# Kernel tuning notes

Measured on AMD Instinct MI355X. Metric: run time of the kernel, lower is better.

Reference implementation:

```python
import jax, jax.numpy as jnp
import numpy as np

NF, NH1, NH21, NH22, NCLS = 6, 128, 128, 128, 3
OBS_X, OBS_Y, OBS_Z, R = 10.0, 10.0, 9.0, 7.0
BATCH = 131072


def setup_inputs() -> dict:
    key = jax.random.key(0)
    ks = jax.random.split(key, 16)
    def lin(kw, kb, fan_in, fan_out):
        bound = 1.0 / np.sqrt(fan_in)
        w = jax.random.uniform(kw, (fan_out, fan_in), jnp.float32, -bound, bound)
        b = jax.random.uniform(kb, (fan_out,), jnp.float32, -bound, bound)
        return w, b
    fc1_w, fc1_b = lin(ks[0], ks[1], NF, NH1)
    fc21_w, fc21_b = lin(ks[2], ks[3], NH1, NH21)
    fc22_w, fc22_b = lin(ks[4], ks[5], NH1, NH22)
    fcm1_w, fcm1_b = lin(ks[6], ks[7], NH21, NH21)
    fcm2_w, fcm2_b = lin(ks[8], ks[9], NH22, NH22)
    fc31_w, fc31_b = lin(ks[10], ks[11], NH21, NCLS)
    fc32_w, fc32_b = lin(ks[12], ks[13], NH22, 2)
    x = jax.random.normal(ks[14], (BATCH, NF), jnp.float32)
    mean = jnp.array([10.0, 0.0, 10.0, 0.0, 9.0, 0.0], jnp.float32)
    std = jnp.array([5.0, 2.0, 5.0, 2.0, 5.0, 2.0], jnp.float32)
    return {"x": x, "mean": mean, "std": std,
            "fc1_w": fc1_w, "fc1_b": fc1_b,
            "fc21_w": fc21_w, "fc21_b": fc21_b,
            "fc22_w": fc22_w, "fc22_b": fc22_b,
            "fcm1_w": fcm1_w, "fcm1_b": fcm1_b,
            "fcm2_w": fcm2_w, "fcm2_b": fcm2_b,
            "fc31_w": fc31_w, "fc31_b": fc31_b,
            "fc32_w": fc32_w, "fc32_b": fc32_b,
            "sgn": 1}


def _forward(x, mean, std, fc1_w, fc1_b, fc21_w, fc21_b, fc22_w, fc22_b,
             fcm1_w, fcm1_b, fcm2_w, fcm2_b, fc31_w, fc31_b, fc32_w, fc32_b):
    x0 = x * std + mean                                   # de-normalized state [B,6]
    h = jnp.tanh(x @ fc1_w.T + fc1_b)                     # [B,NH1]
    x21 = jnp.tanh(h @ fc21_w.T + fc21_b)
    x22 = jnp.tanh(h @ fc22_w.T + fc22_b)
    x21 = jnp.tanh(x21 @ fcm1_w.T + fcm1_b)
    x22 = jnp.tanh(x22 @ fcm2_w.T + fcm2_b)
    x31 = x21 @ fc31_w.T + fc31_b                         # QP linear term p, [B,3]
    x32 = 4.0 * jax.nn.sigmoid(x22 @ fc32_w.T + fc32_b)   # HOCBF penalties, [B,2]

    # higher-order CBF terms
    px, vx, py, vy, pz, vz = (x0[:, i] for i in range(6))
    dx, dy, dz = px - OBS_X, py - OBS_Y, pz - OBS_Z
    barrier = dx**4 + dy**4 + dz**4 - R**4
    barrier_dot = 4.0 * (dx**3 * vx + dy**3 * vy + dz**3 * vz)
    Lf2b = 12.0 * (dx**2 * vx**2 + dy**2 * vy**2 + dz**2 * vz**2)
    G = -4.0 * jnp.stack([dx**3, dy**3, dz**3], axis=-1)  # [B,3], single constraint G u <= h
    hvec = Lf2b + (x32[:, 0] + x32[:, 1]) * barrier_dot + x32[:, 0] * x32[:, 1] * barrier  # [B]

    # QP: min 0.5 u^T u + x31^T u  s.t.  G u <= h  (Q = I, one constraint)
    # Closed-form KKT: u = -x31 - lam*G, lam = max(0, (G @ (-x31) - h) / (G @ G))
    u_unc = -x31
    Gu = jnp.sum(G * u_unc, axis=-1)                      # [B]
    GG = jnp.sum(G * G, axis=-1)                          # [B]
    lam = jnp.maximum(Gu - hvec, 0.0) / GG
    u = u_unc - lam[:, None] * G                          # [B,3]
    return u


def reference(x, mean, std, fc1_w, fc1_b, fc21_w, fc21_b, fc22_w, fc22_b,
              fcm1_w, fcm1_b, fcm2_w, fcm2_b, fc31_w, fc31_b, fc32_w, fc32_b, sgn):
    return _forward(x, mean, std, fc1_w, fc1_b, fc21_w, fc21_b, fc22_w, fc22_b,
                    fcm1_w, fcm1_b, fcm2_w, fcm2_b, fc31_w, fc31_b, fc32_w, fc32_b)
```

## Files before the change

kernel.cpp:

```cpp
#include <hip/hip_runtime.h>

typedef _Float16 half8 __attribute__((ext_vector_type(8)));
typedef _Float16 half4_t __attribute__((ext_vector_type(4)));
typedef __fp16 fp16x2 __attribute__((ext_vector_type(2)));
typedef float float4_t __attribute__((ext_vector_type(4)));
typedef float float2_t __attribute__((ext_vector_type(2)));

#define SB 64
#define NT 512
#define RS (SB * 8)

#define OFF_W1   0
#define OFF_W21  4096
#define OFF_W22  20480
#define OFF_WM1  36864
#define OFF_WM2  53248
#define OFF_W4A  69632
#define OFF_BIAS 73728
#define WS_HELEMS 73728

#define SCL_TANH 2.8853900817779268f
#define SCL_SIG  -1.4426950408889634f

__device__ __forceinline__ float tanh_pre(float a) {
  float e = __builtin_amdgcn_exp2f(a);
  return fmaf(-2.f, __builtin_amdgcn_rcpf(1.f + e), 1.f);
}
__device__ __forceinline__ half4_t pack4(float v0, float v1, float v2, float v3) {
  fp16x2 lo = __builtin_amdgcn_cvt_pkrtz(v0, v1);
  fp16x2 hi = __builtin_amdgcn_cvt_pkrtz(v2, v3);
  half4_t h;
  h[0] = (_Float16)lo[0]; h[1] = (_Float16)lo[1];
  h[2] = (_Float16)hi[0]; h[3] = (_Float16)hi[1];
  return h;
}

__global__ void prepack(const float* __restrict__ w1, const float* __restrict__ w21,
                        const float* __restrict__ w22, const float* __restrict__ wm1,
                        const float* __restrict__ wm2, const float* __restrict__ w31,
                        const float* __restrict__ w32, const float* __restrict__ b1,
                        const float* __restrict__ b21, const float* __restrict__ b22,
                        const float* __restrict__ bm1, const float* __restrict__ bm2,
                        _Float16* __restrict__ ws) {
  const int stride = gridDim.x * blockDim.x;
  for (int i = blockIdx.x * blockDim.x + threadIdx.x; i < WS_HELEMS; i += stride) {
    float v;
    if (i < OFF_W21) {
      int t = i;
      int j = t & 7, c = t >> 3, l16 = c & 15, t1 = c >> 4;
      int k8 = t1 & 3, mt = t1 >> 2;
      int row = mt * 16 + l16, k = k8 * 8 + j;
      v = (k < 6) ? w1[row * 6 + k] * SCL_TANH : 0.f;
    } else if (i < OFF_W4A) {
      int t = i - OFF_W21;
      int m = t >> 14; t &= 16383;
      const float* src = (m == 0) ? w21 : (m == 1) ? w22 : (m == 2) ? wm1 : wm2;
      int j = t & 7, c = t >> 3, l16 = c & 15, t1 = c >> 4;
      int k8 = t1 & 15, mt = t1 >> 4;
      v = src[(mt * 16 + l16) * 128 + k8 * 8 + j] * SCL_TANH;
    } else {
      int t = i - OFF_W4A;
      int j = t & 7, r = t >> 3, l16 = r & 15, q = r >> 4;
      int cc = q & 15, chain = q >> 4;
      int k = cc * 8 + j, m = l16;
      if (chain == 0) v = (m < 3) ? w31[m * 128 + k] : 0.f;
      else            v = (m < 2) ? w32[m * 128 + k] * SCL_SIG : 0.f;
    }
    ws[i] = (_Float16)v;
  }
  float* bws = (float*)(ws + OFF_BIAS);
  for (int i = blockIdx.x * blockDim.x + threadIdx.x; i < 640; i += stride) {
    int layer = i >> 7, idx = i & 127;
    const float* src = (layer == 0) ? b1 : (layer == 1) ? b21
                     : (layer == 2) ? b22 : (layer == 3) ? bm1 : bm2;
    bws[i] = src[idx] * SCL_TANH;
  }
}

__device__ __forceinline__ void layer128(const half8* __restrict__ A, float4_t bv,
                                         const _Float16* __restrict__ inB,
                                         _Float16* __restrict__ outB,
                                         int quad, int l16, int wv) {
  float4_t acc[4];
  acc[0] = bv; acc[1] = bv; acc[2] = bv; acc[3] = bv;
#pragma unroll
  for (int kk = 0; kk < 4; ++kk) {
#pragma unroll
    for (int nt = 0; nt < 4; ++nt) {
      half8 b = *(const half8*)(inB + (kk * 4 + quad) * RS + (nt * 16 + l16) * 8);
      acc[nt] = __builtin_amdgcn_mfma_f32_16x16x32_f16(A[kk], b, acc[nt], 0, 0, 0);
    }
  }
  const int ob = wv * 16 + quad * 4;
  _Float16* base = outB + (ob >> 3) * RS + (ob & 7);
#pragma unroll
  for (int nt = 0; nt < 4; ++nt) {
    const int s = nt * 16 + l16;
    half4_t h = pack4(tanh_pre(acc[nt][0]), tanh_pre(acc[nt][1]),
                      tanh_pre(acc[nt][2]), tanh_pre(acc[nt][3]));
    *(half4_t*)(base + s * 8) = h;
  }
}

__global__ __launch_bounds__(NT, 4) void bnet_main(
    const float* __restrict__ x, const float* __restrict__ meang,
    const float* __restrict__ stdg, const float* __restrict__ b31,
    const float* __restrict__ b32, const _Float16* __restrict__ ws,
    float* __restrict__ out) {
  __shared__ __align__(16) _Float16 bufH[SB * 128];
  __shared__ __align__(16) _Float16 bufA[SB * 128];
  __shared__ __align__(16) _Float16 bufB[SB * 128];
  __shared__ __align__(16) _Float16 bufC[SB * 128];

  const int tid = threadIdx.x;
  const int wv = tid >> 6;
  const int lane = tid & 63;
  const int quad = lane >> 4;
  const int l16 = lane & 15;
  const int s0 = blockIdx.x * SB;
  const float* biasF = (const float*)(ws + OFF_BIAS);
  const int arow = (wv * 16 + quad * 4);

  half8 A1 = *(const half8*)(ws + OFF_W1 + ((wv * 4 + quad) * 16 + l16) * 8);
  float4_t bv1 = *(const float4_t*)(biasF + arow);
  float4_t bv21 = *(const float4_t*)(biasF + 128 + arow);
  float4_t bv22 = *(const float4_t*)(biasF + 256 + arow);
  float4_t bvm1 = *(const float4_t*)(biasF + 384 + arow);
  float4_t bvm2 = *(const float4_t*)(biasF + 512 + arow);
  half8 A21[4];
#pragma unroll
  for (int kk = 0; kk < 4; ++kk)
    A21[kk] = *(const half8*)(ws + OFF_W21 + ((wv * 16 + kk * 4 + quad) * 16 + l16) * 8);

  {
    float4_t acc[4];
    acc[0] = bv1; acc[1] = bv1; acc[2] = bv1; acc[3] = bv1;
#pragma unroll
    for (int nt = 0; nt < 4; ++nt) {
      half8 v;
#pragma unroll
      for (int j = 0; j < 8; ++j) v[j] = (_Float16)0.f;
      if (quad == 0) {
        const float* xp = x + (size_t)(s0 + nt * 16 + l16) * 6;
        float2_t e0 = *(const float2_t*)(xp);
        float2_t e1 = *(const float2_t*)(xp + 2);
        float2_t e2 = *(const float2_t*)(xp + 4);
        v[0] = (_Float16)e0[0]; v[1] = (_Float16)e0[1];
        v[2] = (_Float16)e1[0]; v[3] = (_Float16)e1[1];
        v[4] = (_Float16)e2[0]; v[5] = (_Float16)e2[1];
      }
      acc[nt] = __builtin_amdgcn_mfma_f32_16x16x32_f16(A1, v, acc[nt], 0, 0, 0);
    }
    _Float16* base = bufH + (arow >> 3) * RS + (arow & 7);
#pragma unroll
    for (int nt = 0; nt < 4; ++nt) {
      const int s = nt * 16 + l16;
      half4_t h = pack4(tanh_pre(acc[nt][0]), tanh_pre(acc[nt][1]),
                        tanh_pre(acc[nt][2]), tanh_pre(acc[nt][3]));
      *(half4_t*)(base + s * 8) = h;
    }
  }
  half8 A22[4];
#pragma unroll
  for (int kk = 0; kk < 4; ++kk)
    A22[kk] = *(const half8*)(ws + OFF_W22 + ((wv * 16 + kk * 4 + quad) * 16 + l16) * 8);
  __syncthreads();

  layer128(A21, bv21, bufH, bufA, quad, l16, wv);
  half8 AM1[4];
#pragma unroll
  for (int kk = 0; kk < 4; ++kk)
    AM1[kk] = *(const half8*)(ws + OFF_WM1 + ((wv * 16 + kk * 4 + quad) * 16 + l16) * 8);
  layer128(A22, bv22, bufH, bufB, quad, l16, wv);
  half8 AM2[4];
#pragma unroll
  for (int kk = 0; kk < 4; ++kk)
    AM2[kk] = *(const half8*)(ws + OFF_WM2 + ((wv * 16 + kk * 4 + quad) * 16 + l16) * 8);
  __syncthreads();

  layer128(AM1, bvm1, bufA, bufC, quad, l16, wv);
  half8 A4[2][4];
  if (wv < 4) {
#pragma unroll
    for (int c = 0; c < 2; ++c)
#pragma unroll
      for (int kk = 0; kk < 4; ++kk)
        A4[c][kk] = *(const half8*)(ws + OFF_W4A +
                                    ((c * 16 + kk * 4 + quad) * 16 + l16) * 8);
  }
  layer128(AM2, bvm2, bufB, bufH, quad, l16, wv);
  __syncthreads();

  if (wv < 4) {
    const int nt = wv;
    float4_t c0 = (float4_t){0.f, 0.f, 0.f, 0.f};
    float4_t c1 = (float4_t){0.f, 0.f, 0.f, 0.f};
    if (quad == 0) {
      c0[0] = b31[0]; c0[1] = b31[1]; c0[2] = b31[2];
      c1[0] = b32[0] * SCL_SIG; c1[1] = b32[1] * SCL_SIG;
    }
#pragma unroll
    for (int kk = 0; kk < 4; ++kk) {
      half8 bh = *(const half8*)(bufC + (kk * 4 + quad) * RS + (nt * 16 + l16) * 8);
      half8 bc = *(const half8*)(bufH + (kk * 4 + quad) * RS + (nt * 16 + l16) * 8);
      c0 = __builtin_amdgcn_mfma_f32_16x16x32_f16(A4[0][kk], bh, c0, 0, 0, 0);
      c1 = __builtin_amdgcn_mfma_f32_16x16x32_f16(A4[1][kk], bc, c1, 0, 0, 0);
    }
    if (quad == 0) {
      const int s = nt * 16 + l16;
      float u0 = -c0[0];
      float u1 = -c0[1];
      float u2 = -c0[2];
      float p0 = 4.f * __builtin_amdgcn_rcpf(1.f + __builtin_amdgcn_exp2f(c1[0]));
      float p1 = 4.f * __builtin_amdgcn_rcpf(1.f + __builtin_amdgcn_exp2f(c1[1]));
      const float m0 = meang[0], m1 = meang[1], m2 = meang[2];
      const float m3 = meang[3], m4 = meang[4], m5 = meang[5];
      const float sd0 = stdg[0], sd1 = stdg[1], sd2 = stdg[2];
      const float sd3 = stdg[3], sd4 = stdg[4], sd5 = stdg[5];
      const float* xp = x + (size_t)(s0 + s) * 6;
      float2_t e0 = *(const float2_t*)(xp);
      float2_t e1 = *(const float2_t*)(xp + 2);
      float2_t e2 = *(const float2_t*)(xp + 4);
      float px = e0[0] * sd0 + m0, vx = e0[1] * sd1 + m1;
      float py = e1[0] * sd2 + m2, vy = e1[1] * sd3 + m3;
      float pz = e2[0] * sd4 + m4, vz = e2[1] * sd5 + m5;
      float dx = px - 10.f, dy = py - 10.f, dz = pz - 9.f;
      float dx2 = dx * dx, dy2 = dy * dy, dz2 = dz * dz;
      float dx3 = dx2 * dx, dy3 = dy2 * dy, dz3 = dz2 * dz;
      float barrier = dx3 * dx + dy3 * dy + dz3 * dz - 2401.f;
      float bdot = 4.f * (dx3 * vx + dy3 * vy + dz3 * vz);
      float Lf2b = 12.f * (dx2 * vx * vx + dy2 * vy * vy + dz2 * vz * vz);
      float g0 = -4.f * dx3, g1 = -4.f * dy3, g2 = -4.f * dz3;
      float hv = Lf2b + (p0 + p1) * bdot + p0 * p1 * barrier;
      float Gu = g0 * u0 + g1 * u1 + g2 * u2;
      float GG = g0 * g0 + g1 * g1 + g2 * g2;
      float lam = fmaxf(Gu - hv, 0.f) / GG;
      float* op = out + (size_t)(s0 + s) * 3;
      op[0] = u0 - lam * g0;
      op[1] = u1 - lam * g1;
      op[2] = u2 - lam * g2;
    }
  }
}

extern "C" void kernel_launch(void* const* d_in, const int* in_sizes, int n_in,
                              void* d_out, int out_size, void* d_ws, size_t ws_size,
                              hipStream_t stream) {
  const float* x    = (const float*)d_in[0];
  const float* mean = (const float*)d_in[1];
  const float* stdv = (const float*)d_in[2];
  const float* w1   = (const float*)d_in[3];
  const float* b1   = (const float*)d_in[4];
  const float* w21  = (const float*)d_in[5];
  const float* b21  = (const float*)d_in[6];
  const float* w22  = (const float*)d_in[7];
  const float* b22  = (const float*)d_in[8];
  const float* wm1  = (const float*)d_in[9];
  const float* bm1  = (const float*)d_in[10];
  const float* wm2  = (const float*)d_in[11];
  const float* bm2  = (const float*)d_in[12];
  const float* w31  = (const float*)d_in[13];
  const float* b31  = (const float*)d_in[14];
  const float* w32  = (const float*)d_in[15];
  const float* b32  = (const float*)d_in[16];
  _Float16* ws = (_Float16*)d_ws;
  float* out = (float*)d_out;
  const int batch = in_sizes[0] / 6;

  hipLaunchKernelGGL(prepack, dim3(96), dim3(256), 0, stream,
                     w1, w21, w22, wm1, wm2, w31, w32,
                     b1, b21, b22, bm1, bm2, ws);
  hipLaunchKernelGGL(bnet_main, dim3(batch / SB), dim3(NT), 0, stream,
                     x, mean, stdv, b31, b32, (const _Float16*)ws, out);
}
```

Measured before the change: 120.8 us.

## Keep activations in registers with 32x32 MFMA and per-wave batch tiles

```diff
diff --git a/kernel.cpp b/kernel.cpp
--- a/kernel.cpp
+++ b/kernel.cpp
@@ -1,23 +1,16 @@
 #include <hip/hip_runtime.h>
 
 typedef _Float16 half8 __attribute__((ext_vector_type(8)));
-typedef _Float16 half4_t __attribute__((ext_vector_type(4)));
 typedef __fp16 fp16x2 __attribute__((ext_vector_type(2)));
 typedef float float4_t __attribute__((ext_vector_type(4)));
 typedef float float2_t __attribute__((ext_vector_type(2)));
-
-#define SB 64
-#define NT 512
-#define RS (SB * 8)
-
-#define OFF_W1   0
-#define OFF_W21  4096
-#define OFF_W22  20480
-#define OFF_WM1  36864
-#define OFF_WM2  53248
-#define OFF_W4A  69632
-#define OFF_BIAS 73728
-#define WS_HELEMS 73728
+typedef float float16_t __attribute__((ext_vector_type(16)));
+
+#define OFF_W1 0
+#define OFF_WH 2048
+#define OFF_W4 67584
+#define OFF_BC 75776
+#define WS_HELEMS 75776
 
 #define SCL_TANH 2.8853900817779268f
 #define SCL_SIG  -1.4426950408889634f
@@ -26,13 +19,32 @@
   float e = __builtin_amdgcn_exp2f(a);
   return fmaf(-2.f, __builtin_amdgcn_rcpf(1.f + e), 1.f);
 }
-__device__ __forceinline__ half4_t pack4(float v0, float v1, float v2, float v3) {
-  fp16x2 lo = __builtin_amdgcn_cvt_pkrtz(v0, v1);
-  fp16x2 hi = __builtin_amdgcn_cvt_pkrtz(v2, v3);
-  half4_t h;
-  h[0] = (_Float16)lo[0]; h[1] = (_Float16)lo[1];
-  h[2] = (_Float16)hi[0]; h[3] = (_Float16)hi[1];
-  return h;
+__device__ __forceinline__ float16_t zero16() {
+  float16_t z;
+#pragma unroll
+  for (int i = 0; i < 16; ++i) z[i] = 0.f;
+  return z;
+}
+__device__ __forceinline__ half8 tp8(const float16_t& a, int base,
+                                     float4_t ba, float4_t bb) {
+  fp16x2 p0 = __builtin_amdgcn_cvt_pkrtz(tanh_pre(a[base + 0] + ba[0]),
+                                         tanh_pre(a[base + 1] + ba[1]));
+  fp16x2 p1 = __builtin_amdgcn_cvt_pkrtz(tanh_pre(a[base + 2] + ba[2]),
+                                         tanh_pre(a[base + 3] + ba[3]));
+  fp16x2 p2 = __builtin_amdgcn_cvt_pkrtz(tanh_pre(a[base + 4] + bb[0]),
+                                         tanh_pre(a[base + 5] + bb[1]));
+  fp16x2 p3 = __builtin_amdgcn_cvt_pkrtz(tanh_pre(a[base + 6] + bb[2]),
+                                         tanh_pre(a[base + 7] + bb[3]));
+  half8 r;
+  r[0] = (_Float16)p0[0]; r[1] = (_Float16)p0[1];
+  r[2] = (_Float16)p1[0]; r[3] = (_Float16)p1[1];
+  r[4] = (_Float16)p2[0]; r[5] = (_Float16)p2[1];
+  r[6] = (_Float16)p3[0]; r[7] = (_Float16)p3[1];
+  return r;
+}
+
+__device__ __forceinline__ int kperm(int kc, int hh, int j) {
+  return 32 * (kc >> 1) + 8 * ((kc & 1) * 2 + (j >> 2)) + 4 * hh + (j & 3);
 }
 
 __global__ void prepack(const float* __restrict__ w1, const float* __restrict__ w21,
@@ -45,201 +57,156 @@
   const int stride = gridDim.x * blockDim.x;
   for (int i = blockIdx.x * blockDim.x + threadIdx.x; i < WS_HELEMS; i += stride) {
     float v;
-    if (i < OFF_W21) {
-      int t = i;
-      int j = t & 7, c = t >> 3, l16 = c & 15, t1 = c >> 4;
-      int k8 = t1 & 3, mt = t1 >> 2;
-      int row = mt * 16 + l16, k = k8 * 8 + j;
-      v = (k < 6) ? w1[row * 6 + k] * SCL_TANH : 0.f;
-    } else if (i < OFF_W4A) {
-      int t = i - OFF_W21;
-      int m = t >> 14; t &= 16383;
-      const float* src = (m == 0) ? w21 : (m == 1) ? w22 : (m == 2) ? wm1 : wm2;
-      int j = t & 7, c = t >> 3, l16 = c & 15, t1 = c >> 4;
-      int k8 = t1 & 15, mt = t1 >> 4;
-      v = src[(mt * 16 + l16) * 128 + k8 * 8 + j] * SCL_TANH;
+    if (i < OFF_WH) {
+      int j = i & 7, t = i >> 3, lane = t & 63, mt = t >> 6;
+      int m = mt * 32 + (lane & 31), k = (lane >> 5) * 8 + j;
+      v = (k < 6) ? w1[m * 6 + k] * SCL_TANH
+        : (k == 6) ? b1[m] * SCL_TANH : 0.f;
+    } else if (i < OFF_W4) {
+      int t = i - OFF_WH;
+      int l = t >> 14; t &= 16383;
+      int j = t & 7, t2 = t >> 3, lane = t2 & 63, t3 = t2 >> 6;
+      int mt = t3 & 3, kc = t3 >> 2;
+      int m = mt * 32 + (lane & 31), hh = lane >> 5;
+      int r = kperm(kc, hh, j);
+      const float* src = (l == 0) ? w21 : (l == 1) ? w22 : (l == 2) ? wm1 : wm2;
+      v = src[m * 128 + r] * SCL_TANH;
     } else {
-      int t = i - OFF_W4A;
-      int j = t & 7, r = t >> 3, l16 = r & 15, q = r >> 4;
-      int cc = q & 15, chain = q >> 4;
-      int k = cc * 8 + j, m = l16;
-      if (chain == 0) v = (m < 3) ? w31[m * 128 + k] : 0.f;
-      else            v = (m < 2) ? w32[m * 128 + k] * SCL_SIG : 0.f;
+      int t = i - OFF_W4;
+      int j = t & 7, t2 = t >> 3, lane = t2 & 63, t3 = t2 >> 6;
+      int kc = t3 & 7, c = t3 >> 3;
+      int m = lane & 31, hh = lane >> 5;
+      int r = kperm(kc, hh, j);
+      if (c == 0) v = (m < 3) ? w31[m * 128 + r] : 0.f;
+      else        v = (m < 2) ? w32[m * 128 + r] * SCL_SIG : 0.f;
     }
     ws[i] = (_Float16)v;
   }
-  float* bws = (float*)(ws + OFF_BIAS);
-  for (int i = blockIdx.x * blockDim.x + threadIdx.x; i < 640; i += stride) {
-    int layer = i >> 7, idx = i & 127;
-    const float* src = (layer == 0) ? b1 : (layer == 1) ? b21
-                     : (layer == 2) ? b22 : (layer == 3) ? bm1 : bm2;
-    bws[i] = src[idx] * SCL_TANH;
-  }
-}
-
-__device__ __forceinline__ void layer128(const half8* __restrict__ A, float4_t bv,
-                                         const _Float16* __restrict__ inB,
-                                         _Float16* __restrict__ outB,
-                                         int quad, int l16, int wv) {
-  float4_t acc[4];
-  acc[0] = bv; acc[1] = bv; acc[2] = bv; acc[3] = bv;
-#pragma unroll
-  for (int kk = 0; kk < 4; ++kk) {
-#pragma unroll
-    for (int nt = 0; nt < 4; ++nt) {
-      half8 b = *(const half8*)(inB + (kk * 4 + quad) * RS + (nt * 16 + l16) * 8);
-      acc[nt] = __builtin_amdgcn_mfma_f32_16x16x32_f16(A[kk], b, acc[nt], 0, 0, 0);
-    }
-  }
-  const int ob = wv * 16 + quad * 4;
-  _Float16* base = outB + (ob >> 3) * RS + (ob & 7);
-#pragma unroll
-  for (int nt = 0; nt < 4; ++nt) {
-    const int s = nt * 16 + l16;
-    half4_t h = pack4(tanh_pre(acc[nt][0]), tanh_pre(acc[nt][1]),
-                      tanh_pre(acc[nt][2]), tanh_pre(acc[nt][3]));
-    *(half4_t*)(base + s * 8) = h;
-  }
-}
-
-__global__ __launch_bounds__(NT, 4) void bnet_main(
+  float* bws = (float*)(ws + OFF_BC);
+  for (int i = blockIdx.x * blockDim.x + threadIdx.x; i < 512; i += stride) {
+    int l = i >> 7, t = i & 127, mt = t >> 5, q = t & 31, hh = q >> 4, reg = q & 15;
+    int row = mt * 32 + 8 * (reg >> 2) + 4 * hh + (reg & 3);
+    const float* src = (l == 0) ? b21 : (l == 1) ? b22 : (l == 2) ? bm1 : bm2;
+    bws[i] = src[row] * SCL_TANH;
+  }
+}
+
+__device__ __forceinline__ void hidden(const _Float16* __restrict__ W,
+                                       const float* __restrict__ biasL,
+                                       const half8* __restrict__ Bin,
+                                       half8* __restrict__ Bout, int lo, int hh) {
+  float16_t acc[4];
+#pragma unroll
+  for (int mt = 0; mt < 4; ++mt) acc[mt] = zero16();
+#pragma unroll
+  for (int kc = 0; kc < 8; ++kc) {
+    const _Float16* p = W + kc * 2048 + lo;
+#pragma unroll
+    for (int mt = 0; mt < 4; ++mt) {
+      half8 a = *(const half8*)(p + mt * 512);
+      acc[mt] = __builtin_amdgcn_mfma_f32_32x32x16_f16(a, Bin[kc], acc[mt], 0, 0, 0);
+    }
+  }
+  const float* bp = biasL + hh * 16;
+#pragma unroll
+  for (int mt = 0; mt < 4; ++mt) {
+    float4_t b0 = *(const float4_t*)(bp + mt * 32);
+    float4_t b1v = *(const float4_t*)(bp + mt * 32 + 4);
+    float4_t b2 = *(const float4_t*)(bp + mt * 32 + 8);
+    float4_t b3 = *(const float4_t*)(bp + mt * 32 + 12);
+    Bout[2 * mt]     = tp8(acc[mt], 0, b0, b1v);
+    Bout[2 * mt + 1] = tp8(acc[mt], 8, b2, b3);
+  }
+}
+
+__device__ __forceinline__ float16_t chain8(const _Float16* __restrict__ A,
+                                            const half8* __restrict__ Bin, int lo) {
+  float16_t c = zero16();
+#pragma unroll
+  for (int kc = 0; kc < 8; ++kc) {
+    half8 a = *(const half8*)(A + kc * 512 + lo);
+    c = __builtin_amdgcn_mfma_f32_32x32x16_f16(a, Bin[kc], c, 0, 0, 0);
+  }
+  return c;
+}
+
+__global__ __launch_bounds__(256, 2) void bnet_main(
     const float* __restrict__ x, const float* __restrict__ meang,
     const float* __restrict__ stdg, const float* __restrict__ b31,
     const float* __restrict__ b32, const _Float16* __restrict__ ws,
     float* __restrict__ out) {
-  __shared__ __align__(16) _Float16 bufH[SB * 128];
-  __shared__ __align__(16) _Float16 bufA[SB * 128];
-  __shared__ __align__(16) _Float16 bufB[SB * 128];
-  __shared__ __align__(16) _Float16 bufC[SB * 128];
-
-  const int tid = threadIdx.x;
-  const int wv = tid >> 6;
-  const int lane = tid & 63;
-  const int quad = lane >> 4;
-  const int l16 = lane & 15;
-  const int s0 = blockIdx.x * SB;
-  const float* biasF = (const float*)(ws + OFF_BIAS);
-  const int arow = (wv * 16 + quad * 4);
-
-  half8 A1 = *(const half8*)(ws + OFF_W1 + ((wv * 4 + quad) * 16 + l16) * 8);
-  float4_t bv1 = *(const float4_t*)(biasF + arow);
-  float4_t bv21 = *(const float4_t*)(biasF + 128 + arow);
-  float4_t bv22 = *(const float4_t*)(biasF + 256 + arow);
-  float4_t bvm1 = *(const float4_t*)(biasF + 384 + arow);
-  float4_t bvm2 = *(const float4_t*)(biasF + 512 + arow);
-  half8 A21[4];
-#pragma unroll
-  for (int kk = 0; kk < 4; ++kk)
-    A21[kk] = *(const half8*)(ws + OFF_W21 + ((wv * 16 + kk * 4 + quad) * 16 + l16) * 8);
-
+  const int lane = threadIdx.x & 63;
+  const int hh = lane >> 5;
+  const int s = blockIdx.x * 128 + (threadIdx.x >> 6) * 32 + (lane & 31);
+  const int lo = lane * 8;
+  const float* biasC = (const float*)(ws + OFF_BC);
+
+  float xr0 = 0.f, xr1 = 0.f, xr2 = 0.f, xr3 = 0.f, xr4 = 0.f, xr5 = 0.f;
+  half8 bx;
+#pragma unroll
+  for (int j = 0; j < 8; ++j) bx[j] = (_Float16)0.f;
+  if (hh == 0) {
+    const float* xp = x + (size_t)s * 6;
+    float2_t e0 = *(const float2_t*)(xp);
+    float2_t e1 = *(const float2_t*)(xp + 2);
+    float2_t e2 = *(const float2_t*)(xp + 4);
+    xr0 = e0[0]; xr1 = e0[1]; xr2 = e1[0]; xr3 = e1[1]; xr4 = e2[0]; xr5 = e2[1];
+    bx[0] = (_Float16)xr0; bx[1] = (_Float16)xr1; bx[2] = (_Float16)xr2;
+    bx[3] = (_Float16)xr3; bx[4] = (_Float16)xr4; bx[5] = (_Float16)xr5;
+    bx[6] = (_Float16)1.f;
+  }
+
+  half8 actH[8];
   {
-    float4_t acc[4];
-    acc[0] = bv1; acc[1] = bv1; acc[2] = bv1; acc[3] = bv1;
-#pragma unroll
-    for (int nt = 0; nt < 4; ++nt) {
-      half8 v;
-#pragma unroll
-      for (int j = 0; j < 8; ++j) v[j] = (_Float16)0.f;
-      if (quad == 0) {
-        const float* xp = x + (size_t)(s0 + nt * 16 + l16) * 6;
-        float2_t e0 = *(const float2_t*)(xp);
-        float2_t e1 = *(const float2_t*)(xp + 2);
-        float2_t e2 = *(const float2_t*)(xp + 4);
-        v[0] = (_Float16)e0[0]; v[1] = (_Float16)e0[1];
-        v[2] = (_Float16)e1[0]; v[3] = (_Float16)e1[1];
-        v[4] = (_Float16)e2[0]; v[5] = (_Float16)e2[1];
-      }
-      acc[nt] = __builtin_amdgcn_mfma_f32_16x16x32_f16(A1, v, acc[nt], 0, 0, 0);
-    }
-    _Float16* base = bufH + (arow >> 3) * RS + (arow & 7);
-#pragma unroll
-    for (int nt = 0; nt < 4; ++nt) {
-      const int s = nt * 16 + l16;
-      half4_t h = pack4(tanh_pre(acc[nt][0]), tanh_pre(acc[nt][1]),
-                        tanh_pre(acc[nt][2]), tanh_pre(acc[nt][3]));
-      *(half4_t*)(base + s * 8) = h;
-    }
-  }
-  half8 A22[4];
-#pragma unroll
-  for (int kk = 0; kk < 4; ++kk)
-    A22[kk] = *(const half8*)(ws + OFF_W22 + ((wv * 16 + kk * 4 + quad) * 16 + l16) * 8);
-  __syncthreads();
-
-  layer128(A21, bv21, bufH, bufA, quad, l16, wv);
-  half8 AM1[4];
-#pragma unroll
-  for (int kk = 0; kk < 4; ++kk)
-    AM1[kk] = *(const half8*)(ws + OFF_WM1 + ((wv * 16 + kk * 4 + quad) * 16 + l16) * 8);
-  layer128(A22, bv22, bufH, bufB, quad, l16, wv);
-  half8 AM2[4];
-#pragma unroll
-  for (int kk = 0; kk < 4; ++kk)
-    AM2[kk] = *(const half8*)(ws + OFF_WM2 + ((wv * 16 + kk * 4 + quad) * 16 + l16) * 8);
-  __syncthreads();
-
-  layer128(AM1, bvm1, bufA, bufC, quad, l16, wv);
-  half8 A4[2][4];
-  if (wv < 4) {
-#pragma unroll
-    for (int c = 0; c < 2; ++c)
-#pragma unroll
-      for (int kk = 0; kk < 4; ++kk)
-        A4[c][kk] = *(const half8*)(ws + OFF_W4A +
-                                    ((c * 16 + kk * 4 + quad) * 16 + l16) * 8);
-  }
-  layer128(AM2, bvm2, bufB, bufH, quad, l16, wv);
-  __syncthreads();
-
-  if (wv < 4) {
-    const int nt = wv;
-    float4_t c0 = (float4_t){0.f, 0.f, 0.f, 0.f};
-    float4_t c1 = (float4_t){0.f, 0.f, 0.f, 0.f};
-    if (quad == 0) {
-      c0[0] = b31[0]; c0[1] = b31[1]; c0[2] = b31[2];
-      c1[0] = b32[0] * SCL_SIG; c1[1] = b32[1] * SCL_SIG;
-    }
-#pragma unroll
-    for (int kk = 0; kk < 4; ++kk) {
-      half8 bh = *(const half8*)(bufC + (kk * 4 + quad) * RS + (nt * 16 + l16) * 8);
-      half8 bc = *(const half8*)(bufH + (kk * 4 + quad) * RS + (nt * 16 + l16) * 8);
-      c0 = __builtin_amdgcn_mfma_f32_16x16x32_f16(A4[0][kk], bh, c0, 0, 0, 0);
-      c1 = __builtin_amdgcn_mfma_f32_16x16x32_f16(A4[1][kk], bc, c1, 0, 0, 0);
-    }
-    if (quad == 0) {
-      const int s = nt * 16 + l16;
-      float u0 = -c0[0];
-      float u1 = -c0[1];
-      float u2 = -c0[2];
-      float p0 = 4.f * __builtin_amdgcn_rcpf(1.f + __builtin_amdgcn_exp2f(c1[0]));
-      float p1 = 4.f * __builtin_amdgcn_rcpf(1.f + __builtin_amdgcn_exp2f(c1[1]));
-      const float m0 = meang[0], m1 = meang[1], m2 = meang[2];
-      const float m3 = meang[3], m4 = meang[4], m5 = meang[5];
-      const float sd0 = stdg[0], sd1 = stdg[1], sd2 = stdg[2];
-      const float sd3 = stdg[3], sd4 = stdg[4], sd5 = stdg[5];
-      const float* xp = x + (size_t)(s0 + s) * 6;
-      float2_t e0 = *(const float2_t*)(xp);
-      float2_t e1 = *(const float2_t*)(xp + 2);
-      float2_t e2 = *(const float2_t*)(xp + 4);
-      float px = e0[0] * sd0 + m0, vx = e0[1] * sd1 + m1;
-      float py = e1[0] * sd2 + m2, vy = e1[1] * sd3 + m3;
-      float pz = e2[0] * sd4 + m4, vz = e2[1] * sd5 + m5;
-      float dx = px - 10.f, dy = py - 10.f, dz = pz - 9.f;
-      float dx2 = dx * dx, dy2 = dy * dy, dz2 = dz * dz;
-      float dx3 = dx2 * dx, dy3 = dy2 * dy, dz3 = dz2 * dz;
-      float barrier = dx3 * dx + dy3 * dy + dz3 * dz - 2401.f;
-      float bdot = 4.f * (dx3 * vx + dy3 * vy + dz3 * vz);
-      float Lf2b = 12.f * (dx2 * vx * vx + dy2 * vy * vy + dz2 * vz * vz);
-      float g0 = -4.f * dx3, g1 = -4.f * dy3, g2 = -4.f * dz3;
-      float hv = Lf2b + (p0 + p1) * bdot + p0 * p1 * barrier;
-      float Gu = g0 * u0 + g1 * u1 + g2 * u2;
-      float GG = g0 * g0 + g1 * g1 + g2 * g2;
-      float lam = fmaxf(Gu - hv, 0.f) / GG;
-      float* op = out + (size_t)(s0 + s) * 3;
-      op[0] = u0 - lam * g0;
-      op[1] = u1 - lam * g1;
-      op[2] = u2 - lam * g2;
-    }
+    float16_t a[4];
+#pragma unroll
+    for (int mt = 0; mt < 4; ++mt) {
+      half8 w = *(const half8*)(ws + OFF_W1 + mt * 512 + lo);
+      a[mt] = __builtin_amdgcn_mfma_f32_32x32x16_f16(w, bx, zero16(), 0, 0, 0);
+    }
+    float4_t z4 = (float4_t){0.f, 0.f, 0.f, 0.f};
+#pragma unroll
+    for (int mt = 0; mt < 4; ++mt) {
+      actH[2 * mt]     = tp8(a[mt], 0, z4, z4);
+      actH[2 * mt + 1] = tp8(a[mt], 8, z4, z4);
+    }
+  }
+
+  half8 act21[8], act22[8], actM1[8], actM2[8];
+  hidden(ws + OFF_WH +     0, biasC +   0, actH,  act21, lo, hh);
+  hidden(ws + OFF_WH + 16384, biasC + 128, actH,  act22, lo, hh);
+  hidden(ws + OFF_WH + 32768, biasC + 256, act21, actM1, lo, hh);
+  hidden(ws + OFF_WH + 49152, biasC + 384, act22, actM2, lo, hh);
+
+  float16_t c0 = chain8(ws + OFF_W4,        actM1, lo);
+  float16_t c1 = chain8(ws + OFF_W4 + 4096, actM2, lo);
+
+  if (hh == 0) {
+    float u0 = -(c0[0] + b31[0]);
+    float u1 = -(c0[1] + b31[1]);
+    float u2 = -(c0[2] + b31[2]);
+    float p0 = 4.f * __builtin_amdgcn_rcpf(
+                   1.f + __builtin_amdgcn_exp2f(c1[0] + b32[0] * SCL_SIG));
+    float p1 = 4.f * __builtin_amdgcn_rcpf(
+                   1.f + __builtin_amdgcn_exp2f(c1[1] + b32[1] * SCL_SIG));
+    float px = xr0 * stdg[0] + meang[0], vx = xr1 * stdg[1] + meang[1];
+    float py = xr2 * stdg[2] + meang[2], vy = xr3 * stdg[3] + meang[3];
+    float pz = xr4 * stdg[4] + meang[4], vz = xr5 * stdg[5] + meang[5];
+    float dx = px - 10.f, dy = py - 10.f, dz = pz - 9.f;
+    float dx2 = dx * dx, dy2 = dy * dy, dz2 = dz * dz;
+    float dx3 = dx2 * dx, dy3 = dy2 * dy, dz3 = dz2 * dz;
+    float barrier = dx3 * dx + dy3 * dy + dz3 * dz - 2401.f;
+    float bdot = 4.f * (dx3 * vx + dy3 * vy + dz3 * vz);
+    float Lf2b = 12.f * (dx2 * vx * vx + dy2 * vy * vy + dz2 * vz * vz);
+    float g0 = -4.f * dx3, g1 = -4.f * dy3, g2 = -4.f * dz3;
+    float hv = Lf2b + (p0 + p1) * bdot + p0 * p1 * barrier;
+    float Gu = g0 * u0 + g1 * u1 + g2 * u2;
+    float GG = g0 * g0 + g1 * g1 + g2 * g2;
+    float lam = fmaxf(Gu - hv, 0.f) / GG;
+    float* op = out + (size_t)s * 3;
+    op[0] = u0 - lam * g0;
+    op[1] = u1 - lam * g1;
+    op[2] = u2 - lam * g2;
   }
 }
 
@@ -270,6 +237,6 @@
   hipLaunchKernelGGL(prepack, dim3(96), dim3(256), 0, stream,
                      w1, w21, w22, wm1, wm2, w31, w32,
                      b1, b21, b22, bm1, bm2, ws);
-  hipLaunchKernelGGL(bnet_main, dim3(batch / SB), dim3(NT), 0, stream,
+  hipLaunchKernelGGL(bnet_main, dim3(batch / 128), dim3(256), 0, stream,
                      x, mean, stdv, b31, b32, (const _Float16*)ws, out);
 }
```

New measurement: 156.5 us. 1.3x slower.
